# Kernel tuning notes

Measured on AMD Instinct MI355X. Metric: run time of the kernel, lower is better.

Reference implementation:

```python
import jax, jax.numpy as jnp
import numpy as np

SH_BASE = 0.28209479177387814
T_THRESH = 1e-4


def quat_to_rot(q):
    # q: [N,4] (w,x,y,z) -> [N,3,3]
    q = q / jnp.linalg.norm(q, axis=-1, keepdims=True)
    w, x, y, z = q[..., 0], q[..., 1], q[..., 2], q[..., 3]
    return jnp.stack([
        jnp.stack([1 - 2 * (y * y + z * z), 2 * (x * y - w * z), 2 * (x * z + w * y)], -1),
        jnp.stack([2 * (x * y + w * z), 1 - 2 * (x * x + z * z), 2 * (y * z - w * x)], -1),
        jnp.stack([2 * (x * z - w * y), 2 * (y * z + w * x), 1 - 2 * (x * x + y * y)], -1),
    ], -2)


def setup_inputs() -> dict:
    key = jax.random.key(0)
    ks = jax.random.split(key, 6)
    N, H, W = 1024, 256, 256
    u = jax.random.uniform(ks[0], (N, 3))
    z = 2.0 + 6.0 * u[:, 2]  # depths in [2,8], in front of camera
    mean = jnp.stack([(u[:, 0] * 2 - 1) * 0.6 * z, (u[:, 1] * 2 - 1) * 0.6 * z, z], -1)
    qvec = jnp.concatenate([jnp.ones((N, 1)), 0.1 * jax.random.normal(ks[1], (N, 3))], -1)
    svec_b = jnp.log(0.03) + 0.3 * jax.random.normal(ks[2], (N, 3))  # exp-activated scales
    sh = 0.5 * jax.random.normal(ks[3], (N, 3, 9))  # sh_order=3 -> 9 coeffs, only DC used (now_C=1)
    alpha_b = -2.0 + 0.5 * jax.random.normal(ks[4], (N,))  # sigmoid-activated opacity ~0.1
    c2w = jnp.eye(4, dtype=jnp.float32)
    return dict(mean=mean, qvec=qvec, svec_before_activation=svec_b, sh_coeffs=sh,
                alpha_before_activation=alpha_b, c2w=c2w, H=H, W=W)


def reference(mean, qvec, svec_before_activation, sh_coeffs, alpha_before_activation, c2w, H, W):
    fx = float(W); fy = float(W); cx = W / 2.0; cy = H / 2.0
    Rw = c2w[:3, :3].T  # world->camera rotation
    t = c2w[:3, 3]
    p = (mean - t) @ Rw.T  # [N,3] camera-space points
    z = jnp.maximum(p[:, 2], 1e-3)
    # depth sort (front to back), as done by tile_culling_aabb_start_end
    order = jnp.argsort(z)
    p = p[order]; z = z[order]
    qvec = qvec[order]; sb = svec_before_activation[order]
    sh = sh_coeffs[order]; ab = alpha_before_activation[order]
    x, y = p[:, 0], p[:, 1]
    mx, my = x / z, y / z  # projected 2D mean on normalized image plane
    svec = jnp.exp(sb)
    alpha = jax.nn.sigmoid(ab)
    Rq = quat_to_rot(qvec)
    M = Rq * svec[:, None, :]
    cov3d = M @ M.transpose(0, 2, 1)  # [N,3,3]
    cov_cam = jnp.einsum('ij,njk,lk->nil', Rw, cov3d, Rw)
    iz = 1.0 / z; iz2 = iz * iz
    zeros = jnp.zeros_like(iz)
    J = jnp.stack([jnp.stack([iz, zeros, -x * iz2], -1),
                   jnp.stack([zeros, iz, -y * iz2], -1)], -2)  # [N,2,3]
    cov2d = jnp.einsum('nij,njk,nlk->nil', J, cov_cam, J)  # [N,2,2]
    a = cov2d[:, 0, 0] + 1e-8; b = cov2d[:, 0, 1]; c = cov2d[:, 1, 1] + 1e-8
    det = a * c - b * b
    ia, ib, ic = c / det, -b / det, a / det  # inverse 2x2 covariance
    # pixel centers on the normalized image plane
    tlx = -cx / fx; tly = -cy / fy; psx = 1.0 / fx; psy = 1.0 / fy
    px = tlx + (jnp.arange(W, dtype=jnp.float32) + 0.5) * psx  # [W]
    py = tly + (jnp.arange(H, dtype=jnp.float32) + 0.5) * psy  # [H]
    dx = px[None, :] - mx[:, None]  # [N,W]
    dy = py[None, :] - my[:, None]  # [N,H]
    quad = (ia[:, None, None] * (dx * dx)[:, None, :]
            + 2.0 * ib[:, None, None] * dy[:, :, None] * dx[:, None, :]
            + ic[:, None, None] * (dy * dy)[:, :, None])  # [N,H,W]
    G = jnp.exp(-0.5 * quad)
    w = (alpha[:, None, None] * G).reshape(G.shape[0], -1)  # [N,P]
    logw = jnp.log1p(-jnp.clip(w, 0.0, 0.9999))
    cT = jnp.cumsum(logw, axis=0)
    T = jnp.exp(jnp.concatenate([jnp.zeros_like(cT[:1]), cT[:-1]], 0))  # exclusive transmittance
    contrib = jnp.where(T > T_THRESH, w * T, 0.0)  # early termination below T_thresh
    color = jax.nn.sigmoid(SH_BASE * sh[:, :, 0])  # DC SH -> rgb, [N,3]
    out = jnp.einsum('np,nc->pc', contrib, color)
    return out.reshape(H, W, 3)
```

## Files before the change

kernel.cpp:

```cpp
#include <hip/hip_runtime.h>

#define IMG_H 256
#define IMG_W 256
#define NG 1024
#define SH_BASE_F 0.28209479177387814f
#define L2E 1.4426950408889634f
#define LOG2EPS -26.575424759098898f

__global__ __launch_bounds__(256) void fused_render_kernel(
    const float* __restrict__ mean,
    const float* __restrict__ qvec,
    const float* __restrict__ svecb,
    const float* __restrict__ shc,
    const float* __restrict__ alphab,
    const float* __restrict__ c2w,
    float* __restrict__ out,
    int N)
{
    __shared__ float4 comp[NG][2];
    __shared__ ulonglong2 skey2[NG / 2];
    __shared__ int wcnt[4];
    unsigned long long* skey = (unsigned long long*)skey2;

    const int tid = threadIdx.x;
    const int row = blockIdx.x;
    const float py = ((float)row + 0.5f - (float)IMG_H * 0.5f) / (float)IMG_W;
    const int wlane = tid & 63;
    const int wid = tid >> 6;
    const unsigned long long lanemask = (1ull << wlane) - 1ull;

    float C[16];
#pragma unroll
    for (int k = 0; k < 16; ++k) C[k] = c2w[k];
    const float t0 = C[3], t1 = C[7], t2 = C[11];
    const float Rw00 = C[0], Rw01 = C[4], Rw02 = C[8];
    const float Rw10 = C[1], Rw11 = C[5], Rw12 = C[9];
    const float Rw20 = C[2], Rw21 = C[6], Rw22 = C[10];

    int cnt = 0;
    for (int r = 0; r < 4; ++r) {
        const int n = r * 256 + tid;
        bool keep = false;
        float mx = 0.f, qa = 0.f, B = 0.f, Cc = 0.f, cr = 0.f, cg = 0.f, cb = 0.f;
        unsigned long long zk = 0;
        if (n < N) {
            const float d0 = mean[3 * n + 0] - t0;
            const float d1 = mean[3 * n + 1] - t1;
            const float d2 = mean[3 * n + 2] - t2;
            const float p0 = Rw00 * d0 + Rw01 * d1 + Rw02 * d2;
            const float p1 = Rw10 * d0 + Rw11 * d1 + Rw12 * d2;
            const float p2 = Rw20 * d0 + Rw21 * d1 + Rw22 * d2;

            const float z  = fmaxf(p2, 0.001f);
            const float iz = 1.0f / z;
            mx = p0 * iz;
            const float my = p1 * iz;

            float qw = qvec[4 * n + 0];
            float qx = qvec[4 * n + 1];
            float qy = qvec[4 * n + 2];
            float qz = qvec[4 * n + 3];
            const float qinv = 1.0f / sqrtf(qw * qw + qx * qx + qy * qy + qz * qz);
            qw *= qinv; qx *= qinv; qy *= qinv; qz *= qinv;
            const float R00 = 1.f - 2.f * (qy * qy + qz * qz);
            const float R01 = 2.f * (qx * qy - qw * qz);
            const float R02 = 2.f * (qx * qz + qw * qy);
            const float R10 = 2.f * (qx * qy + qw * qz);
            const float R11 = 1.f - 2.f * (qx * qx + qz * qz);
            const float R12 = 2.f * (qy * qz - qw * qx);
            const float R20 = 2.f * (qx * qz - qw * qy);
            const float R21 = 2.f * (qy * qz + qw * qx);
            const float R22 = 1.f - 2.f * (qx * qx + qy * qy);

            const float s0 = expf(svecb[3 * n + 0]);
            const float s1 = expf(svecb[3 * n + 1]);
            const float s2 = expf(svecb[3 * n + 2]);

            const float M00 = R00 * s0, M01 = R01 * s1, M02 = R02 * s2;
            const float M10 = R10 * s0, M11 = R11 * s1, M12 = R12 * s2;
            const float M20 = R20 * s0, M21 = R21 * s1, M22 = R22 * s2;
            const float V00 = M00 * M00 + M01 * M01 + M02 * M02;
            const float V01 = M00 * M10 + M01 * M11 + M02 * M12;
            const float V02 = M00 * M20 + M01 * M21 + M02 * M22;
            const float V11 = M10 * M10 + M11 * M11 + M12 * M12;
            const float V12 = M10 * M20 + M11 * M21 + M12 * M22;
            const float V22 = M20 * M20 + M21 * M21 + M22 * M22;

            const float A00 = Rw00 * V00 + Rw01 * V01 + Rw02 * V02;
            const float A01 = Rw00 * V01 + Rw01 * V11 + Rw02 * V12;
            const float A02 = Rw00 * V02 + Rw01 * V12 + Rw02 * V22;
            const float A10 = Rw10 * V00 + Rw11 * V01 + Rw12 * V02;
            const float A11 = Rw10 * V01 + Rw11 * V11 + Rw12 * V12;
            const float A12 = Rw10 * V02 + Rw11 * V12 + Rw12 * V22;
            const float A20 = Rw20 * V00 + Rw21 * V01 + Rw22 * V02;
            const float A21 = Rw20 * V01 + Rw21 * V11 + Rw22 * V12;
            const float A22 = Rw20 * V02 + Rw21 * V12 + Rw22 * V22;
            const float CC00 = A00 * Rw00 + A01 * Rw01 + A02 * Rw02;
            const float CC01 = A00 * Rw10 + A01 * Rw11 + A02 * Rw12;
            const float CC02 = A00 * Rw20 + A01 * Rw21 + A02 * Rw22;
            const float CC11 = A10 * Rw10 + A11 * Rw11 + A12 * Rw12;
            const float CC12 = A10 * Rw20 + A11 * Rw21 + A12 * Rw22;
            const float CC22 = A20 * Rw20 + A21 * Rw21 + A22 * Rw22;

            const float iz2 = iz * iz;
            const float j02 = -p0 * iz2, j12 = -p1 * iz2;
            const float T00 = iz * CC00 + j02 * CC02;
            const float T01 = iz * CC01 + j02 * CC12;
            const float T02 = iz * CC02 + j02 * CC22;
            const float T11 = iz * CC11 + j12 * CC12;
            const float T12 = iz * CC12 + j12 * CC22;
            const float c2d00 = T00 * iz + T02 * j02;
            const float c2d01 = T01 * iz + T02 * j12;
            const float c2d11 = T11 * iz + T12 * j12;

            const float a = c2d00 + 1e-8f;
            const float b = c2d01;
            const float c = c2d11 + 1e-8f;
            const float idet = 1.0f / (a * c - b * b);
            const float ia = c * idet, ib = -b * idet, ic = a * idet;

            qa = -0.5f * ia * L2E;
            const float qb = -ib * L2E;
            const float qc = -0.5f * ic * L2E;
            const float alpha = 1.0f / (1.0f + expf(-alphab[n]));
            const float la = log2f(alpha);
            cr = 1.0f / (1.0f + expf(-SH_BASE_F * shc[27 * n + 0]));
            cg = 1.0f / (1.0f + expf(-SH_BASE_F * shc[27 * n + 9]));
            cb = 1.0f / (1.0f + expf(-SH_BASE_F * shc[27 * n + 18]));

            const float dy = py - my;
            B  = qb * dy;
            Cc = fmaf(qc * dy, dy, la);
            const float pmax = Cc - (B * B) / (4.0f * qa);
            keep = (pmax > LOG2EPS);
            zk = ((unsigned long long)__float_as_uint(z) << 32) | (unsigned)n;
        }

        const unsigned long long mask = __ballot(keep);
        if (wlane == 0) wcnt[wid] = __popcll(mask);
        __syncthreads();
        int base = cnt;
#pragma unroll
        for (int w = 0; w < 4; ++w) base += (w < wid) ? wcnt[w] : 0;
        if (keep) {
            const int slot = base + __popcll(mask & lanemask);
            comp[slot][0] = make_float4(mx, qa, B, Cc);
            comp[slot][1] = make_float4(cr, cg, cb, 0.f);
            skey[slot] = zk;
        }
        cnt += wcnt[0] + wcnt[1] + wcnt[2] + wcnt[3];
        __syncthreads();
    }

    const int M = cnt;
    const int pad = (32 - (M & 31)) & 31;
    if (tid < pad) {
        comp[M + tid][0] = make_float4(0.f, 0.f, 0.f, -1000.f);
        comp[M + tid][1] = make_float4(0.f, 0.f, 0.f, 0.f);
        skey[M + tid] = 0xFFFFFFFF00000000ull | (unsigned)(M + tid);
    }
    __syncthreads();
    const int Mp = M + pad;

    float4 sr0[4], sr1[4];
    int srk[4];
#pragma unroll
    for (int q = 0; q < 4; ++q) {
        const int s = q * 256 + tid;
        if (s < Mp) {
            const unsigned long long k = skey[s];
            int rank = 0;
            for (int jb = 0; jb < (Mp >> 1); ++jb) {
                const ulonglong2 kk = skey2[jb];
                rank += (kk.x < k) ? 1 : 0;
                rank += (kk.y < k) ? 1 : 0;
            }
            sr0[q] = comp[s][0];
            sr1[q] = comp[s][1];
            srk[q] = rank;
        }
    }
    __syncthreads();
#pragma unroll
    for (int q = 0; q < 4; ++q) {
        const int s = q * 256 + tid;
        if (s < Mp) {
            comp[srk[q]][0] = sr0[q];
            comp[srk[q]][1] = sr1[q];
        }
    }
    __syncthreads();

    const float px = ((float)tid + 0.5f - (float)IMG_W * 0.5f) / (float)IMG_W;
    float T = 1.0f;
    float ar = 0.f, ag = 0.f, ab = 0.f;
    for (int mb = 0; mb < Mp; mb += 32) {
#pragma unroll 8
        for (int k = 0; k < 32; ++k) {
            const int m = mb + k;
            const float4 c0 = comp[m][0];
            const float4 c1 = comp[m][1];
            const float dx = px - c0.x;
            const float p  = fmaf(dx, fmaf(c0.y, dx, c0.z), c0.w);
            const float w  = __builtin_amdgcn_exp2f(p);
            const float wT = w * T;
            ar = fmaf(wT, c1.x, ar);
            ag = fmaf(wT, c1.y, ag);
            ab = fmaf(wT, c1.z, ab);
            T = fmaf(-fminf(w, 0.9999f), T, T);
        }
        if (__all(T <= 0.0001f)) break;
    }

    const int o = (row * IMG_W + tid) * 3;
    out[o + 0] = ar;
    out[o + 1] = ag;
    out[o + 2] = ab;
}

extern "C" void kernel_launch(void* const* d_in, const int* in_sizes, int n_in,
                              void* d_out, int out_size, void* d_ws, size_t ws_size,
                              hipStream_t stream)
{
    const float* mean   = (const float*)d_in[0];
    const float* qvec   = (const float*)d_in[1];
    const float* svecb  = (const float*)d_in[2];
    const float* shc    = (const float*)d_in[3];
    const float* alphab = (const float*)d_in[4];
    const float* c2w    = (const float*)d_in[5];

    const int N = in_sizes[0] / 3;

    fused_render_kernel<<<IMG_H, 256, 0, stream>>>(
        mean, qvec, svecb, shc, alphab, c2w, (float*)d_out, N);
}
```

Before: 78.71 us.

## Add cheap conservative row pre-cull before full per-Gaussian setup

Result: faster. 76.23 us (-3.2%).

```diff
diff --git a/kernel.cpp b/kernel.cpp
--- a/kernel.cpp
+++ b/kernel.cpp
@@ -6,6 +6,7 @@
 #define SH_BASE_F 0.28209479177387814f
 #define L2E 1.4426950408889634f
 #define LOG2EPS -26.575424759098898f
+#define PRECULL_K 37.5f
 
 __global__ __launch_bounds__(256) void fused_render_kernel(
     const float* __restrict__ mean,
@@ -19,15 +20,17 @@
 {
     __shared__ float4 comp[NG][2];
     __shared__ ulonglong2 skey2[NG / 2];
-    __shared__ int wcnt[4];
+    __shared__ int idxbuf[NG];
+    __shared__ int cntp, cnt;
     unsigned long long* skey = (unsigned long long*)skey2;
 
     const int tid = threadIdx.x;
     const int row = blockIdx.x;
     const float py = ((float)row + 0.5f - (float)IMG_H * 0.5f) / (float)IMG_W;
     const int wlane = tid & 63;
-    const int wid = tid >> 6;
     const unsigned long long lanemask = (1ull << wlane) - 1ull;
+
+    if (tid == 0) { cntp = 0; cnt = 0; }
 
     float C[16];
 #pragma unroll
@@ -37,13 +40,46 @@
     const float Rw10 = C[1], Rw11 = C[5], Rw12 = C[9];
     const float Rw20 = C[2], Rw21 = C[6], Rw22 = C[10];
 
-    int cnt = 0;
+    __syncthreads();
+
+#pragma unroll
     for (int r = 0; r < 4; ++r) {
         const int n = r * 256 + tid;
+        bool keepp = false;
+        if (n < N) {
+            const float d0 = mean[3 * n + 0] - t0;
+            const float d1 = mean[3 * n + 1] - t1;
+            const float d2 = mean[3 * n + 2] - t2;
+            const float p1 = Rw10 * d0 + Rw11 * d1 + Rw12 * d2;
+            const float p2 = Rw20 * d0 + Rw21 * d1 + Rw22 * d2;
+            const float z  = fmaxf(p2, 0.001f);
+            const float iz = 1.0f / z;
+            const float my = p1 * iz;
+            const float dy = py - my;
+            const float sb0 = svecb[3 * n + 0];
+            const float sb1 = svecb[3 * n + 1];
+            const float sb2 = svecb[3 * n + 2];
+            const float s2max = expf(2.0f * fmaxf(fmaxf(sb0, sb1), sb2));
+            const float cub = iz * iz * fmaf(my, my, 1.0f) * s2max + 1e-8f;
+            keepp = (dy * dy <= PRECULL_K * cub);
+        }
+        const unsigned long long m = __ballot(keepp);
+        int base = 0;
+        if (wlane == 0) base = atomicAdd(&cntp, __popcll(m));
+        base = __shfl(base, 0);
+        if (keepp) idxbuf[base + __popcll(m & lanemask)] = n;
+    }
+    __syncthreads();
+    const int Mpre = cntp;
+
+    const int rounds = (Mpre + 255) >> 8;
+    for (int q = 0; q < rounds; ++q) {
+        const int s = q * 256 + tid;
         bool keep = false;
         float mx = 0.f, qa = 0.f, B = 0.f, Cc = 0.f, cr = 0.f, cg = 0.f, cb = 0.f;
         unsigned long long zk = 0;
-        if (n < N) {
+        if (s < Mpre) {
+            const int n = idxbuf[s];
             const float d0 = mean[3 * n + 0] - t0;
             const float d1 = mean[3 * n + 1] - t1;
             const float d2 = mean[3 * n + 2] - t2;
@@ -56,10 +92,8 @@
             mx = p0 * iz;
             const float my = p1 * iz;
 
-            float qw = qvec[4 * n + 0];
-            float qx = qvec[4 * n + 1];
-            float qy = qvec[4 * n + 2];
-            float qz = qvec[4 * n + 3];
+            const float4 q4 = ((const float4*)qvec)[n];
+            float qw = q4.x, qx = q4.y, qy = q4.z, qz = q4.w;
             const float qinv = 1.0f / sqrtf(qw * qw + qx * qx + qy * qy + qz * qz);
             qw *= qinv; qx *= qinv; qy *= qinv; qz *= qinv;
             const float R00 = 1.f - 2.f * (qy * qy + qz * qz);
@@ -136,21 +170,18 @@
             zk = ((unsigned long long)__float_as_uint(z) << 32) | (unsigned)n;
         }
 
-        const unsigned long long mask = __ballot(keep);
-        if (wlane == 0) wcnt[wid] = __popcll(mask);
-        __syncthreads();
-        int base = cnt;
-#pragma unroll
-        for (int w = 0; w < 4; ++w) base += (w < wid) ? wcnt[w] : 0;
+        const unsigned long long m = __ballot(keep);
+        int base = 0;
+        if (wlane == 0) base = atomicAdd(&cnt, __popcll(m));
+        base = __shfl(base, 0);
         if (keep) {
-            const int slot = base + __popcll(mask & lanemask);
+            const int slot = base + __popcll(m & lanemask);
             comp[slot][0] = make_float4(mx, qa, B, Cc);
             comp[slot][1] = make_float4(cr, cg, cb, 0.f);
             skey[slot] = zk;
         }
-        cnt += wcnt[0] + wcnt[1] + wcnt[2] + wcnt[3];
-        __syncthreads();
-    }
+    }
+    __syncthreads();
 
     const int M = cnt;
     const int pad = (32 - (M & 31)) & 31;
```
